# Kernel optimization log

Hardware: AMD Instinct MI355X
Metric: run time of the kernel (lower is better)

The kernel has to match this reference:

```python
import jax, jax.numpy as jnp
import numpy as np

CHEB_K = 3


def cheb_gcn(x, node_emb, w_pool, b_pool):
    # x: [B, N, C], node_emb: [N, D], w_pool: [D, K, C, O], b_pool: [D, O]
    n = node_emb.shape[0]
    A = jax.nn.softmax(jax.nn.relu(node_emb @ node_emb.T), axis=1)  # [N, N]
    supports = [jnp.eye(n, dtype=x.dtype), A]
    for _ in range(2, CHEB_K):
        supports.append(2.0 * A @ supports[-1] - supports[-2])
    S = jnp.stack(supports, axis=0)  # [K, N, N]
    weights = jnp.einsum('nd,dkio->nkio', node_emb, w_pool)  # [N, K, C, O]
    bias = node_emb @ b_pool  # [N, O]
    x_g = jnp.einsum('knm,bmc->bnkc', S, x)  # [B, N, K, C]
    return jnp.einsum('bnki,nkio->bno', x_g, weights) + bias


def setup_inputs() -> dict:
    key = jax.random.key(0)
    ks = jax.random.split(key, 7)
    B, N, DIN, DOUT, E = 64, 1024, 64, 64, 16
    C = DIN + DOUT
    return {
        'x': jax.random.normal(ks[0], (B, N, DIN), jnp.float32),
        'state': jax.random.normal(ks[1], (B, N, DOUT), jnp.float32),
        'node_embeddings': jax.random.normal(ks[2], (N, E), jnp.float32),
        'W_gate': jax.random.normal(ks[3], (E, CHEB_K, C, 2 * DOUT), jnp.float32) * 0.1,
        'b_gate': jax.random.normal(ks[4], (E, 2 * DOUT), jnp.float32) * 0.1,
        'W_update': jax.random.normal(ks[5], (E, CHEB_K, C, DOUT), jnp.float32) * 0.1,
        'b_update': jax.random.normal(ks[6], (E, DOUT), jnp.float32) * 0.1,
    }


def reference(x, state, node_embeddings, W_gate, b_gate, W_update, b_update):
    hidden = state.shape[-1]
    inp = jnp.concatenate([x, state], axis=-1)  # [B, N, DIN+DOUT]
    z_r = jax.nn.sigmoid(cheb_gcn(inp, node_embeddings, W_gate, b_gate))
    z, r = z_r[..., :hidden], z_r[..., hidden:]
    cand = jnp.concatenate([x, r * state], axis=-1)
    h_hat = jnp.tanh(cheb_gcn(cand, node_embeddings, W_update, b_update))
    return z * state + (1.0 - z) * h_hat
```

## Files before the change

### kernel.cpp

```cpp
#include <hip/hip_runtime.h>
#include <hip/hip_bf16.h>
#include <math.h>

#define B_ 64
#define N_ 1024
#define E_ 16

typedef unsigned short ushort_t;
typedef __attribute__((ext_vector_type(8))) short bf16x8;
typedef __attribute__((ext_vector_type(4))) float f32x4;

__device__ __forceinline__ float sigmoidf_(float x) {
  return 1.0f / (1.0f + __expf(-x));
}
__device__ __forceinline__ ushort_t f2bf(float f) {
  unsigned int u = __float_as_uint(f);
  u = (u + 0x7fffu + ((u >> 16) & 1u)) >> 16;
  return (ushort_t)u;
}
__device__ __forceinline__ float bf2f(ushort_t h) { return __uint_as_float((unsigned)h << 16); }
__device__ __forceinline__ void gload16(const void* g, void* l) {
  __builtin_amdgcn_global_load_lds(
      (const __attribute__((address_space(1))) unsigned int*)g,
      (__attribute__((address_space(3))) unsigned int*)l, 16, 0, 0);
}

__global__ __launch_bounds__(256) void compute_A_kernel(const float* __restrict__ emb,
                                                        ushort_t* __restrict__ Ah,
                                                        ushort_t* __restrict__ Al) {
  __shared__ float embn[E_];
  __shared__ float red[256];
  const int n = blockIdx.x;
  const int t = threadIdx.x;
  if (t < E_) embn[t] = emb[n * E_ + t];
  __syncthreads();
  float s[4];
#pragma unroll
  for (int j = 0; j < 4; ++j) {
    const int m = j * 256 + t;
    const float* em = emb + m * E_;
    float acc = 0.f;
#pragma unroll
    for (int d = 0; d < E_; ++d) acc = fmaf(embn[d], em[d], acc);
    s[j] = fmaxf(acc, 0.f);
  }
  float mx = fmaxf(fmaxf(s[0], s[1]), fmaxf(s[2], s[3]));
  red[t] = mx;
  __syncthreads();
  for (int off = 128; off > 0; off >>= 1) {
    if (t < off) red[t] = fmaxf(red[t], red[t + off]);
    __syncthreads();
  }
  mx = red[0];
  __syncthreads();
  float e[4], lsum = 0.f;
#pragma unroll
  for (int j = 0; j < 4; ++j) { e[j] = __expf(s[j] - mx); lsum += e[j]; }
  red[t] = lsum;
  __syncthreads();
  for (int off = 128; off > 0; off >>= 1) {
    if (t < off) red[t] += red[t + off];
    __syncthreads();
  }
  const float inv = 1.0f / red[0];
#pragma unroll
  for (int j = 0; j < 4; ++j) {
    const float v = e[j] * inv;
    ushort_t h = f2bf(v);
    Ah[n * N_ + j * 256 + t] = h;
    Al[n * N_ + j * 256 + t] = f2bf(v - bf2f(h));
  }
}

__global__ __launch_bounds__(256) void transpose_A_kernel(const ushort_t* __restrict__ src1,
                                                          ushort_t* __restrict__ dst1,
                                                          const ushort_t* __restrict__ src2,
                                                          ushort_t* __restrict__ dst2) {
  __shared__ ushort_t tile[128][130];
  const int t = threadIdx.x;
  const int r0 = blockIdx.y << 7, c0 = blockIdx.x << 7;
  const ushort_t* src = src1;
  ushort_t* dst = dst1;
#pragma unroll
  for (int p = 0; p < 2; ++p) {
    if (p) { src = src2; dst = dst2; __syncthreads(); }
#pragma unroll
    for (int it = 0; it < 8; ++it) {
      const int id = it * 256 + t;
      const int row = id >> 4, ch = (id & 15) << 3;
      *(uint4*)&tile[row][ch] = *(const uint4*)&src[(size_t)(r0 + row) * 1024 + c0 + ch];
    }
    __syncthreads();
#pragma unroll
    for (int it = 0; it < 8; ++it) {
      const int id = it * 256 + t;
      const int row = id >> 4, ch = (id & 15) << 3;
      ushort_t v[8];
#pragma unroll
      for (int u = 0; u < 8; ++u) v[u] = tile[ch + u][row];
      *(uint4*)&dst[(size_t)(c0 + row) * 1024 + r0 + ch] = *(const uint4*)v;
    }
    __syncthreads();
  }
}

__global__ __launch_bounds__(256) void build_T0t_kernel(const float* __restrict__ xA,
                                                        const float* __restrict__ xB,
                                                        ushort_t* __restrict__ Th,
                                                        ushort_t* __restrict__ Tl) {
  __shared__ float tile[128][129];
  const int t = threadIdx.x;
  const int b = blockIdx.y;
  const int n0 = blockIdx.x << 7;
  const int c4 = (t & 31) << 2, nl = t >> 5;
#pragma unroll
  for (int p = 0; p < 16; ++p) {
    const int n = nl + (p << 3);
    const float4 v = (c4 < 64)
        ? *(const float4*)&xA[((size_t)b << 16) + ((size_t)(n0 + n) << 6) + c4]
        : *(const float4*)&xB[((size_t)b << 16) + ((size_t)(n0 + n) << 6) + c4 - 64];
    tile[c4 + 0][n] = v.x; tile[c4 + 1][n] = v.y;
    tile[c4 + 2][n] = v.z; tile[c4 + 3][n] = v.w;
  }
  __syncthreads();
  const int c = t >> 1, nc = (t & 1) << 6;
  const size_t obase = ((size_t)(b << 7) + c) * 1024 + n0 + nc;
#pragma unroll
  for (int u = 0; u < 64; u += 4) {
    ushort4 h, l;
    float v0 = tile[c][nc + u + 0], v1 = tile[c][nc + u + 1];
    float v2 = tile[c][nc + u + 2], v3 = tile[c][nc + u + 3];
    h.x = f2bf(v0); l.x = f2bf(v0 - bf2f(h.x));
    h.y = f2bf(v1); l.y = f2bf(v1 - bf2f(h.y));
    h.z = f2bf(v2); l.z = f2bf(v2 - bf2f(h.z));
    h.w = f2bf(v3); l.w = f2bf(v3 - bf2f(h.w));
    *(ushort4*)&Th[obase + u] = h;
    *(ushort4*)&Tl[obase + u] = l;
  }
}

__global__ __launch_bounds__(256) void build_T0s_kernel(const float* __restrict__ rs,
                                                        ushort_t* __restrict__ Th,
                                                        ushort_t* __restrict__ Tl) {
  __shared__ float tile[64][129];
  const int t = threadIdx.x;
  const int b = blockIdx.y;
  const int n0 = blockIdx.x << 7;
  const int c4 = (t & 15) << 2, nl = t >> 4;
#pragma unroll
  for (int p = 0; p < 8; ++p) {
    const int n = nl + (p << 4);
    const float4 v = *(const float4*)&rs[((size_t)b << 16) + ((size_t)(n0 + n) << 6) + c4];
    tile[c4 + 0][n] = v.x; tile[c4 + 1][n] = v.y;
    tile[c4 + 2][n] = v.z; tile[c4 + 3][n] = v.w;
  }
  __syncthreads();
  const int c = t >> 2, nc = (t & 3) << 5;
  const size_t obase = ((size_t)(b << 6) + c) * 1024 + n0 + nc;
#pragma unroll
  for (int u = 0; u < 32; u += 4) {
    ushort4 h, l;
    float v0 = tile[c][nc + u + 0], v1 = tile[c][nc + u + 1];
    float v2 = tile[c][nc + u + 2], v3 = tile[c][nc + u + 3];
    h.x = f2bf(v0); l.x = f2bf(v0 - bf2f(h.x));
    h.y = f2bf(v1); l.y = f2bf(v1 - bf2f(h.y));
    h.z = f2bf(v2); l.z = f2bf(v2 - bf2f(h.z));
    h.w = f2bf(v3); l.w = f2bf(v3 - bf2f(h.w));
    *(ushort4*)&Th[obase + u] = h;
    *(ushort4*)&Tl[obase + u] = l;
  }
}

template <int MODE, int SPAN>
__global__ __launch_bounds__(256, 2) void mfma_gemm_kernel(
    const ushort_t* __restrict__ Ah, const ushort_t* __restrict__ Al,
    const ushort_t* __restrict__ Bh, const ushort_t* __restrict__ Bl,
    ushort_t* __restrict__ OutH, ushort_t* __restrict__ OutL) {
  __shared__ ushort_t smem[2 * 4 * 4096];
  const int t = threadIdx.x;
  const int wave = t >> 6, lane = t & 63;
  const int n0 = blockIdx.y << 7;
  const int bcol = blockIdx.x;
  const int j0 = bcol << 7;
  const int wr = wave >> 1, wc = wave & 1;
  const int fr = lane & 15, fq = lane >> 4;

  f32x4 acc[4][4];
#pragma unroll
  for (int i = 0; i < 4; ++i)
#pragma unroll
    for (int j = 0; j < 4; ++j) acc[i][j] = (f32x4){0.f, 0.f, 0.f, 0.f};

  const int lr3 = lane >> 3;
  const int cs = (lane & 7) ^ lr3;
  const int rofs = (cs >> 2);
  const int kkofs = (cs & 3) << 3;
  auto STAGE = [&](int bsel, int kb) {
#pragma unroll
    for (int i = 0; i < 2; ++i) {
      const int q = (wave << 1) + i;
      const int v = (q << 3) + lr3;
      const int r = (v << 1) + rofs;
      const int lo = bsel * 16384 + q * 512 + lane * 8;
      const size_t ga = (size_t)(n0 + r) * 1024 + kb + kkofs;
      const size_t gb = (size_t)(j0 + r) * 1024 + kb + kkofs;
      gload16(Ah + ga, smem + lo);
      gload16(Al + ga, smem + 4096 + lo);
      gload16(Bh + gb, smem + 8192 + lo);
      gload16(Bl + gb, smem + 12288 + lo);
    }
  };
  auto FRAG = [&](const ushort_t* arrbase, int r) -> bf16x8 {
    const int v = r >> 1;
    const int b = ((((r & 1) << 2) | fq) ^ (v & 7)) << 4;
    return *(const bf16x8*)((const char*)arrbase + v * 128 + b);
  };

  STAGE(0, 0);
  __syncthreads();
  for (int k = 0; k < 32; ++k) {
    if (k < 31) STAGE((k + 1) & 1, (k + 1) << 5);
    const ushort_t* cb = smem + (k & 1) * 16384;
    bf16x8 ah[4], al[4], bh[4], bl[4];
#pragma unroll
    for (int mi = 0; mi < 4; ++mi) {
      const int r = (wr << 6) + (mi << 4) + fr;
      ah[mi] = FRAG(cb, r);
      al[mi] = FRAG(cb + 4096, r);
    }
#pragma unroll
    for (int nj = 0; nj < 4; ++nj) {
      const int r = (wc << 6) + (nj << 4) + fr;
      bh[nj] = FRAG(cb + 8192, r);
      bl[nj] = FRAG(cb + 12288, r);
    }
#pragma unroll
    for (int mi = 0; mi < 4; ++mi)
#pragma unroll
      for (int nj = 0; nj < 4; ++nj) {
        acc[mi][nj] = __builtin_amdgcn_mfma_f32_16x16x32_bf16(ah[mi], bh[nj], acc[mi][nj], 0, 0, 0);
        acc[mi][nj] = __builtin_amdgcn_mfma_f32_16x16x32_bf16(ah[mi], bl[nj], acc[mi][nj], 0, 0, 0);
        acc[mi][nj] = __builtin_amdgcn_mfma_f32_16x16x32_bf16(al[mi], bh[nj], acc[mi][nj], 0, 0, 0);
      }
    __syncthreads();
  }

  ushort_t* hiT = smem;
  ushort_t* loT = smem + 16384;
#pragma unroll
  for (int mi = 0; mi < 4; ++mi) {
    const int nl = (wr << 6) + (mi << 4) + (fq << 2);
#pragma unroll
    for (int nj = 0; nj < 4; ++nj) {
      const int jl = (wc << 6) + (nj << 4) + fr;
      const f32x4 vv = acc[mi][nj];
#pragma unroll
      for (int r = 0; r < 4; ++r) {
        const float v = (MODE == 1) ? 2.0f * vv[r] : vv[r];
        const ushort_t h = f2bf(v);
        hiT[(nl + r) * 128 + jl] = h;
        loT[(nl + r) * 128 + jl] = f2bf(v - bf2f(h));
      }
    }
  }
  __syncthreads();
  const int soff = (n0 >= 1024) ? 128 : 0;
  const int n0e = n0 & 1023;
#pragma unroll
  for (int rr = 0; rr < 8; ++rr) {
    const int id = rr * 256 + t;
    const int nl = id >> 4, ch = id & 15;
    size_t dstE;
    if (MODE == 1) {
      dstE = (size_t)(n0 + nl) * 1024 + j0 + ch * 8;
    } else if (SPAN == 128) {
      dstE = ((size_t)(n0e + nl) * 64 + bcol) * 256 + soff + ch * 8;
    } else {
      const int bb = bcol * 2 + (ch >> 3);
      dstE = ((size_t)(n0e + nl) * 64 + bb) * 256 + soff + 64 + (ch & 7) * 8;
    }
    *(uint4*)&OutH[dstE] = *(const uint4*)((const char*)hiT + nl * 256 + ch * 16);
    *(uint4*)&OutL[dstE] = *(const uint4*)((const char*)loT + nl * 256 + ch * 16);
  }
}

template <int OW>
__global__ __launch_bounds__(256) void wpt_kernel(const float* __restrict__ Wp,
                                                  float* __restrict__ WpT) {
  const int idx = blockIdx.x * 256 + threadIdx.x;
  const int ki = idx % 384;
  const int k = ki >> 7, i = ki & 127;
  const int o = idx / 384;
  float v[16];
#pragma unroll
  for (int d = 0; d < 16; ++d) v[d] = Wp[((size_t)d * 384 + ki) * OW + o];
  if (k == 0) {
#pragma unroll
    for (int d = 0; d < 16; ++d) v[d] -= Wp[((size_t)d * 384 + 256 + i) * OW + o];
  }
  float* dst = WpT + (size_t)idx * 16;
#pragma unroll
  for (int q = 0; q < 4; ++q) *(float4*)&dst[q * 4] = *(const float4*)&v[q * 4];
}

__global__ __launch_bounds__(384) void wcombine5_kernel(const float* __restrict__ emb,
                                                        const float* __restrict__ WpT,
                                                        ushort_t* __restrict__ WtH,
                                                        ushort_t* __restrict__ WtL) {
  __shared__ float embs[256 * 16];
  __shared__ ushort_t sH[8 * 384];
  __shared__ ushort_t sL[8 * 384];
  const int t = threadIdx.x;
  const int o = blockIdx.y;
  const int n0 = blockIdx.x << 8;
  for (int i = t; i < 1024; i += 384)
    *(float4*)&embs[i * 4] = *(const float4*)&emb[(size_t)n0 * 16 + i * 4];
  float wreg[16];
  {
    const float* src = WpT + (size_t)o * 6144 + t * 16;
#pragma unroll
    for (int q = 0; q < 4; ++q) *(float4*)&wreg[q * 4] = *(const float4*)&src[q * 4];
  }
  __syncthreads();
  for (int g = 0; g < 32; ++g) {
#pragma unroll
    for (int nl = 0; nl < 8; ++nl) {
      const float* e = &embs[(g * 8 + nl) * 16];
      float a = 0.f;
#pragma unroll
      for (int d = 0; d < 16; ++d) a = fmaf(e[d], wreg[d], a);
      const ushort_t h = f2bf(a);
      sH[nl * 384 + t] = h;
      sL[nl * 384 + t] = f2bf(a - bf2f(h));
    }
    __syncthreads();
    const size_t ob = ((size_t)o * 1024 + n0 + g * 8) * 384 + t * 8;
    *(uint4*)&WtH[ob] = *(const uint4*)&sH[t * 8];
    *(uint4*)&WtL[ob] = *(const uint4*)&sL[t * 8];
    __syncthreads();
  }
}

template <int MODE>
__global__ __launch_bounds__(256, 2) void pernode_mfma_kernel(
    const float* __restrict__ xA, const float* __restrict__ xB,
    const ushort_t* __restrict__ XpH, const ushort_t* __restrict__ XpL,
    const ushort_t* __restrict__ WtH, const ushort_t* __restrict__ WtL,
    const float* __restrict__ emb, const float* __restrict__ bsrc, int bstride,
    const float* __restrict__ state, const float* __restrict__ zb,
    float* __restrict__ dst) {
  __shared__ ushort_t xh_s[64 * 128];
  __shared__ ushort_t xl_s[64 * 128];
  __shared__ ushort_t wh_s[64 * 128];
  __shared__ ushort_t wl_s[64 * 128];
  __shared__ float embn[E_];
  __shared__ float bias[64];
  const int n = blockIdx.x;
  const int t = threadIdx.x;
  if (t < E_) embn[t] = emb[n * E_ + t];
  __syncthreads();
  if (t < 64) {
    float a = 0.f;
#pragma unroll
    for (int d = 0; d < E_; ++d) a = fmaf(embn[d], bsrc[d * bstride + t], a);
    bias[t] = a;
  }
  const int wave = t >> 6, lane = t & 63;
  const int fr = lane & 15, fq = lane >> 4;
  f32x4 acc[4];
#pragma unroll
  for (int i = 0; i < 4; ++i) acc[i] = (f32x4){0.f, 0.f, 0.f, 0.f};

#pragma unroll
  for (int s = 0; s < 3; ++s) {
    __syncthreads();
    if (s == 0) {
      const int b = t >> 2, q = t & 3;
      const float* srcp = (q < 2)
          ? xA + ((size_t)b << 16) + ((size_t)n << 6) + (q << 5)
          : xB + ((size_t)b << 16) + ((size_t)n << 6) + ((q - 2) << 5);
      float v[32];
#pragma unroll
      for (int j = 0; j < 8; ++j) *(float4*)&v[j * 4] = *(const float4*)&srcp[j * 4];
      const int swz = (b & 7) << 4;
#pragma unroll
      for (int jc = 0; jc < 4; ++jc) {
        unsigned int hh[4], ll[4];
#pragma unroll
        for (int e = 0; e < 4; ++e) {
          const float a0 = v[jc * 8 + 2 * e], a1 = v[jc * 8 + 2 * e + 1];
          const ushort_t h0 = f2bf(a0), h1 = f2bf(a1);
          const ushort_t l0 = f2bf(a0 - bf2f(h0)), l1 = f2bf(a1 - bf2f(h1));
          hh[e] = (unsigned)h0 | ((unsigned)h1 << 16);
          ll[e] = (unsigned)l0 | ((unsigned)l1 << 16);
        }
        const int dstb = b * 256 + (((q << 6) + (jc << 4)) ^ swz);
        *(uint4*)((char*)xh_s + dstb) = make_uint4(hh[0], hh[1], hh[2], hh[3]);
        *(uint4*)((char*)xl_s + dstb) = make_uint4(ll[0], ll[1], ll[2], ll[3]);
      }
    } else {
#pragma unroll
      for (int r = 0; r < 4; ++r) {
        const int id = r * 256 + t;
        const int row = id >> 4, ch = id & 15;
        const int selem = (((ch << 4) ^ ((row & 7) << 4)) >> 1);
        const size_t so = ((size_t)n * 64 + row) * 256 + (s - 1) * 128 + selem;
        gload16(XpH + so, xh_s + id * 8);
        gload16(XpL + so, xl_s + id * 8);
      }
    }
#pragma unroll
    for (int r = 0; r < 4; ++r) {
      const int id = r * 256 + t;
      const int row = id >> 4, ch = id & 15;
      const int selem = (((ch << 4) ^ ((row & 7) << 4)) >> 1);
      const size_t so = ((size_t)row * 1024 + n) * 384 + s * 128 + selem;
      gload16(WtH + so, wh_s + id * 8);
      gload16(WtL + so, wl_s + id * 8);
    }
    __syncthreads();
#pragma unroll
    for (int ks = 0; ks < 4; ++ks) {
      bf16x8 ah[4], al[4];
#pragma unroll
      for (int mi = 0; mi < 4; ++mi) {
        const int r = (mi << 4) + fr;
        const int kb = ((ks << 6) + (fq << 4)) ^ ((r & 7) << 4);
        ah[mi] = *(const bf16x8*)((const char*)xh_s + r * 256 + kb);
        al[mi] = *(const bf16x8*)((const char*)xl_s + r * 256 + kb);
      }
      const int rw = (wave << 4) + fr;
      const int kbw = ((ks << 6) + (fq << 4)) ^ ((rw & 7) << 4);
      const bf16x8 wh = *(const bf16x8*)((const char*)wh_s + rw * 256 + kbw);
      const bf16x8 wl = *(const bf16x8*)((const char*)wl_s + rw * 256 + kbw);
#pragma unroll
      for (int mi = 0; mi < 4; ++mi) {
        acc[mi] = __builtin_amdgcn_mfma_f32_16x16x32_bf16(ah[mi], wh, acc[mi], 0, 0, 0);
        acc[mi] = __builtin_amdgcn_mfma_f32_16x16x32_bf16(al[mi], wh, acc[mi], 0, 0, 0);
        acc[mi] = __builtin_amdgcn_mfma_f32_16x16x32_bf16(ah[mi], wl, acc[mi], 0, 0, 0);
      }
    }
  }

  const int o = (wave << 4) + fr;
  const float bia = bias[o];
#pragma unroll
  for (int mi = 0; mi < 4; ++mi) {
    const int b0 = (mi << 4) + (fq << 2);
    const f32x4 vv = acc[mi];
#pragma unroll
    for (int r = 0; r < 4; ++r) {
      const int b = b0 + r;
      const size_t base = ((size_t)b << 16) + ((size_t)n << 6);
      const float a = vv[r] + bia;
      if (MODE == 0) {
        dst[base + o] = sigmoidf_(a);
      } else if (MODE == 1) {
        dst[base + o] = sigmoidf_(a) * state[base + o];
      } else {
        const float z = zb[base + o], st = state[base + o];
        dst[base + o] = z * st + (1.f - z) * tanhf(a);
      }
    }
  }
}

extern "C" void kernel_launch(void* const* d_in, const int* in_sizes, int n_in,
                              void* d_out, int out_size, void* d_ws, size_t ws_size,
                              hipStream_t stream) {
  const float* x     = (const float*)d_in[0];
  const float* state = (const float*)d_in[1];
  const float* emb   = (const float*)d_in[2];
  const float* Wg    = (const float*)d_in[3];
  const float* bg    = (const float*)d_in[4];
  const float* Wu    = (const float*)d_in[5];
  const float* bu    = (const float*)d_in[6];
  float* out = (float*)d_out;

  char* w = (char*)d_ws;
  ushort_t* AhS  = (ushort_t*)(w);
  ushort_t* AlS  = (ushort_t*)(w + ((size_t)4 << 20));
  ushort_t* Ath  = (ushort_t*)(w + ((size_t)8 << 20));
  ushort_t* Atl  = (ushort_t*)(w + ((size_t)10 << 20));
  ushort_t* T0th = (ushort_t*)(w + ((size_t)12 << 20));
  ushort_t* T0tl = (ushort_t*)(w + ((size_t)28 << 20));
  ushort_t* XpH  = (ushort_t*)(w + ((size_t)44 << 20));
  ushort_t* XpL  = (ushort_t*)(w + ((size_t)76 << 20));
  ushort_t* WtH  = (ushort_t*)(w + ((size_t)108 << 20));
  ushort_t* WtL  = (ushort_t*)(w + ((size_t)156 << 20));
  float*    rs   = (float*)(w + ((size_t)204 << 20));
  float*    WpTg = (float*)(w + ((size_t)220 << 20));
  float*    WpTu = (float*)(w + ((size_t)223 << 20));
  ushort_t* Mh = AhS + (size_t)1024 * 1024;
  ushort_t* Ml = AlS + (size_t)1024 * 1024;
  float* zb = out;

  const dim3 ggd(64, 16);
  const dim3 gud(32, 16);
  const dim3 gm(8, 8);
  const dim3 gt(8, 64);
  const dim3 gc(4, 64);

  compute_A_kernel<<<N_, 256, 0, stream>>>(emb, AhS, AlS);
  transpose_A_kernel<<<gm, 256, 0, stream>>>(AhS, Ath, AlS, Atl);
  mfma_gemm_kernel<1, 128><<<gm, 256, 0, stream>>>(AhS, AlS, Ath, Atl, Mh, Ml);
  wpt_kernel<128><<<192, 256, 0, stream>>>(Wg, WpTg);
  wpt_kernel<64><<<96, 256, 0, stream>>>(Wu, WpTu);

  build_T0t_kernel<<<gt, 256, 0, stream>>>(x, state, T0th, T0tl);
  mfma_gemm_kernel<0, 128><<<ggd, 256, 0, stream>>>(AhS, AlS, T0th, T0tl, XpH, XpL);
  wcombine5_kernel<<<gc, 384, 0, stream>>>(emb, WpTg, WtH, WtL);
  pernode_mfma_kernel<0><<<N_, 256, 0, stream>>>(x, state, XpH, XpL, WtH, WtL, emb, bg, 128,
                                                 state, nullptr, zb);
  wcombine5_kernel<<<gc, 384, 0, stream>>>(emb, WpTg + (size_t)64 * 6144, WtH, WtL);
  pernode_mfma_kernel<1><<<N_, 256, 0, stream>>>(x, state, XpH, XpL, WtH, WtL, emb, bg + 64, 128,
                                                 state, nullptr, rs);

  wcombine5_kernel<<<gc, 384, 0, stream>>>(emb, WpTu, WtH, WtL);
  build_T0s_kernel<<<gt, 256, 0, stream>>>(rs, T0th, T0tl);
  mfma_gemm_kernel<0, 64><<<gud, 256, 0, stream>>>(AhS, AlS, T0th, T0tl, XpH, XpL);
  pernode_mfma_kernel<2><<<N_, 256, 0, stream>>>(x, rs, XpH, XpL, WtH, WtL, emb, bu, 64,
                                                 state, zb, out);
}
```

Measured before the change: 481.9 us.

## Single-buffer GEMM LDS to raise occupancy to four blocks per CU

Halves the shared-memory footprint of the MFMA GEMM kernel by dropping the double-buffered K-loop staging in favour of a single buffer with syncs around each load. The hi and lo bf16 epilogue outputs are now written in two passes through the same tile. Launch bounds are raised to 4 blocks per CU so more waves can hide latency. In exchange, global loads no longer overlap with MFMA compute inside a block, and there are extra barriers. The 4-blocks-per-CU bound may also force register spills with the 4x4 accumulator array.

```diff
diff --git a/kernel.cpp b/kernel.cpp
--- a/kernel.cpp
+++ b/kernel.cpp
@@ -172,11 +172,11 @@
 }
 
 template <int MODE, int SPAN>
-__global__ __launch_bounds__(256, 2) void mfma_gemm_kernel(
+__global__ __launch_bounds__(256, 4) void mfma_gemm_kernel(
     const ushort_t* __restrict__ Ah, const ushort_t* __restrict__ Al,
     const ushort_t* __restrict__ Bh, const ushort_t* __restrict__ Bl,
     ushort_t* __restrict__ OutH, ushort_t* __restrict__ OutL) {
-  __shared__ ushort_t smem[2 * 4 * 4096];
+  __shared__ ushort_t smem[4 * 4096];
   const int t = threadIdx.x;
   const int wave = t >> 6, lane = t & 63;
   const int n0 = blockIdx.y << 7;
@@ -195,13 +195,13 @@
   const int cs = (lane & 7) ^ lr3;
   const int rofs = (cs >> 2);
   const int kkofs = (cs & 3) << 3;
-  auto STAGE = [&](int bsel, int kb) {
+  auto STAGE = [&](int kb) {
 #pragma unroll
     for (int i = 0; i < 2; ++i) {
       const int q = (wave << 1) + i;
       const int v = (q << 3) + lr3;
       const int r = (v << 1) + rofs;
-      const int lo = bsel * 16384 + q * 512 + lane * 8;
+      const int lo = q * 512 + lane * 8;
       const size_t ga = (size_t)(n0 + r) * 1024 + kb + kkofs;
       const size_t gb = (size_t)(j0 + r) * 1024 + kb + kkofs;
       gload16(Ah + ga, smem + lo);
@@ -216,23 +216,22 @@
     return *(const bf16x8*)((const char*)arrbase + v * 128 + b);
   };
 
-  STAGE(0, 0);
-  __syncthreads();
   for (int k = 0; k < 32; ++k) {
-    if (k < 31) STAGE((k + 1) & 1, (k + 1) << 5);
-    const ushort_t* cb = smem + (k & 1) * 16384;
+    __syncthreads();
+    STAGE(k << 5);
+    __syncthreads();
     bf16x8 ah[4], al[4], bh[4], bl[4];
 #pragma unroll
     for (int mi = 0; mi < 4; ++mi) {
       const int r = (wr << 6) + (mi << 4) + fr;
-      ah[mi] = FRAG(cb, r);
-      al[mi] = FRAG(cb + 4096, r);
+      ah[mi] = FRAG(smem, r);
+      al[mi] = FRAG(smem + 4096, r);
     }
 #pragma unroll
     for (int nj = 0; nj < 4; ++nj) {
       const int r = (wc << 6) + (nj << 4) + fr;
-      bh[nj] = FRAG(cb + 8192, r);
-      bl[nj] = FRAG(cb + 12288, r);
+      bh[nj] = FRAG(smem + 8192, r);
+      bl[nj] = FRAG(smem + 12288, r);
     }
 #pragma unroll
     for (int mi = 0; mi < 4; ++mi)
@@ -242,45 +241,46 @@
         acc[mi][nj] = __builtin_amdgcn_mfma_f32_16x16x32_bf16(ah[mi], bl[nj], acc[mi][nj], 0, 0, 0);
         acc[mi][nj] = __builtin_amdgcn_mfma_f32_16x16x32_bf16(al[mi], bh[nj], acc[mi][nj], 0, 0, 0);
       }
-    __syncthreads();
-  }
-
-  ushort_t* hiT = smem;
-  ushort_t* loT = smem + 16384;
-#pragma unroll
-  for (int mi = 0; mi < 4; ++mi) {
-    const int nl = (wr << 6) + (mi << 4) + (fq << 2);
-#pragma unroll
-    for (int nj = 0; nj < 4; ++nj) {
-      const int jl = (wc << 6) + (nj << 4) + fr;
-      const f32x4 vv = acc[mi][nj];
-#pragma unroll
-      for (int r = 0; r < 4; ++r) {
-        const float v = (MODE == 1) ? 2.0f * vv[r] : vv[r];
-        const ushort_t h = f2bf(v);
-        hiT[(nl + r) * 128 + jl] = h;
-        loT[(nl + r) * 128 + jl] = f2bf(v - bf2f(h));
-      }
-    }
-  }
-  __syncthreads();
+  }
+
+  ushort_t* tileT = smem;
   const int soff = (n0 >= 1024) ? 128 : 0;
   const int n0e = n0 & 1023;
 #pragma unroll
-  for (int rr = 0; rr < 8; ++rr) {
-    const int id = rr * 256 + t;
-    const int nl = id >> 4, ch = id & 15;
-    size_t dstE;
-    if (MODE == 1) {
-      dstE = (size_t)(n0 + nl) * 1024 + j0 + ch * 8;
-    } else if (SPAN == 128) {
-      dstE = ((size_t)(n0e + nl) * 64 + bcol) * 256 + soff + ch * 8;
-    } else {
-      const int bb = bcol * 2 + (ch >> 3);
-      dstE = ((size_t)(n0e + nl) * 64 + bb) * 256 + soff + 64 + (ch & 7) * 8;
-    }
-    *(uint4*)&OutH[dstE] = *(const uint4*)((const char*)hiT + nl * 256 + ch * 16);
-    *(uint4*)&OutL[dstE] = *(const uint4*)((const char*)loT + nl * 256 + ch * 16);
+  for (int ph = 0; ph < 2; ++ph) {
+    __syncthreads();
+#pragma unroll
+    for (int mi = 0; mi < 4; ++mi) {
+      const int nl = (wr << 6) + (mi << 4) + (fq << 2);
+#pragma unroll
+      for (int nj = 0; nj < 4; ++nj) {
+        const int jl = (wc << 6) + (nj << 4) + fr;
+        const f32x4 vv = acc[mi][nj];
+#pragma unroll
+        for (int r = 0; r < 4; ++r) {
+          const float v = (MODE == 1) ? 2.0f * vv[r] : vv[r];
+          const ushort_t h = f2bf(v);
+          tileT[(nl + r) * 128 + jl] = ph ? f2bf(v - bf2f(h)) : h;
+        }
+      }
+    }
+    __syncthreads();
+    ushort_t* Out = ph ? OutL : OutH;
+#pragma unroll
+    for (int rr = 0; rr < 8; ++rr) {
+      const int id = rr * 256 + t;
+      const int nl = id >> 4, ch = id & 15;
+      size_t dstE;
+      if (MODE == 1) {
+        dstE = (size_t)(n0 + nl) * 1024 + j0 + ch * 8;
+      } else if (SPAN == 128) {
+        dstE = ((size_t)(n0e + nl) * 64 + bcol) * 256 + soff + ch * 8;
+      } else {
+        const int bb = bcol * 2 + (ch >> 3);
+        dstE = ((size_t)(n0e + nl) * 64 + bb) * 256 + soff + 64 + (ch & 7) * 8;
+      }
+      *(uint4*)&Out[dstE] = *(const uint4*)((const char*)tileT + nl * 256 + ch * 16);
+    }
   }
 }
 
```

Result: slower. 550.6 us (+14.3%).
